# Optimization experiments

Hardware: AMD Instinct MI355X
Metric: run time of the kernel (lower is better)

Reference implementation:

```python
import jax, jax.numpy as jnp
import numpy as np
import math

B, L, DP, DB, H, DH = 1, 256, 128, 128, 8, 32


def _ln(x, g, b, eps=1e-5):
    m = x.mean(-1, keepdims=True)
    v = x.var(-1, keepdims=True)
    return (x - m) / jnp.sqrt(v + eps) * g + b


def setup_inputs() -> dict:
    key = jax.random.key(0)
    ks = jax.random.split(key, 12)
    s_in = 1.0 / math.sqrt(DP)
    s_hd = 1.0 / math.sqrt(H * DH)
    return {
        "pair": jax.random.normal(ks[0], (B, L, L, DP), jnp.float32),
        "bias": jax.random.normal(ks[1], (B, L, L, DB), jnp.float32),
        "mask": jax.random.randint(ks[2], (B, L), 0, 2, jnp.int32),
        "g_pair": jnp.ones((DP,), jnp.float32),
        "b_pair": jnp.zeros((DP,), jnp.float32),
        "g_bias": jnp.ones((DB,), jnp.float32),
        "b_bias": jnp.zeros((DB,), jnp.float32),
        "Wq": jax.random.normal(ks[3], (DP, H * DH), jnp.float32) * s_in,
        "Wk": jax.random.normal(ks[4], (DP, H * DH), jnp.float32) * s_in,
        "Wv": jax.random.normal(ks[5], (DP, H * DH), jnp.float32) * s_in,
        "Wb": jax.random.normal(ks[6], (DB, H), jnp.float32) * s_in,
        "Wg": jax.random.normal(ks[7], (DP, H * DH), jnp.float32) * s_in,
        "bg": jnp.ones((H * DH,), jnp.float32),
        "Wo": jax.random.normal(ks[8], (H * DH, DP), jnp.float32) * s_hd,
        "bo": jnp.zeros((DP,), jnp.float32),
    }


def reference(pair, bias, mask, g_pair, b_pair, g_bias, b_bias,
              Wq, Wk, Wv, Wb, Wg, bg, Wo, bo):
    is_row = True
    scaling = 1.0 / math.sqrt(DH)

    mask_b = (mask == 0)                               # [B,L], True = masked
    mask_2d = mask_b[:, None, :] | mask_b[:, :, None]  # [B,L,L]

    p = jnp.nan_to_num(pair)
    bi = jnp.nan_to_num(bias)
    if is_row:
        p = p.transpose(0, 2, 1, 3)
        bi = bi.transpose(0, 2, 1, 3)
        mask_2d = mask_2d.transpose(0, 2, 1)

    pn = _ln(p, g_pair, b_pair)        # [B,L,L,DP]
    bn = _ln(bi, g_bias, b_bias)       # [B,L,L,DB]

    q = (pn @ Wq).reshape(B, L, L, H, DH) * scaling
    k = (pn @ Wk).reshape(B, L, L, H, DH) / math.sqrt(L)
    v = (pn @ Wv).reshape(B, L, L, H, DH)
    b_proj = bn @ Wb                   # [B,L,L,H]
    gate = jax.nn.sigmoid(pn @ Wg + bg)  # [B,L,L,H*DH]

    # scores summed over the axial (n) axis AND head dim k
    attn = jnp.einsum('bnihk,bnjhk->bijh', q, k) + b_proj
    attn = jnp.where(mask_2d[..., None], -1e9, attn)
    attn = jax.nn.softmax(attn, axis=-2)  # over j

    out = jnp.einsum('bijh,bkjhd->bikhd', attn, v).reshape(B, L, L, H * DH)
    out = gate * out
    out = out @ Wo + bo                # [B,L,L,DP]
    if is_row:
        out = out.transpose(0, 2, 1, 3)
    # note: faithful to source — output mask uses the (permuted) mask_2d frame
    out = jnp.where(mask_2d[..., None], 0.0, out)
    return out
```

## Files before the change

kernel.cpp:

```cpp
#include <hip/hip_runtime.h>
#include <math.h>


typedef unsigned short u16;
typedef __attribute__((ext_vector_type(8))) short short8;
typedef __attribute__((ext_vector_type(4))) short short4v;
typedef __attribute__((ext_vector_type(4))) float float4v;

__device__ __forceinline__ u16 f2bf(float f) {
  unsigned int u = __float_as_uint(f);
  u += 0x7FFFu + ((u >> 16) & 1u);
  return (u16)(u >> 16);
}
__device__ __forceinline__ float bf2f(u16 h) {
  return __uint_as_float(((unsigned int)h) << 16);
}

__global__ __launch_bounds__(256, 4) void k_pre(
    const float* __restrict__ x1, const float* __restrict__ g1,
    const float* __restrict__ b1, u16* __restrict__ y1,
    const float* __restrict__ x2, const float* __restrict__ g2,
    const float* __restrict__ b2, const float* __restrict__ Wb,
    float* __restrict__ Bp,
    const float* __restrict__ Wq, const float* __restrict__ Wk,
    const float* __restrict__ Wv, const float* __restrict__ Wg,
    const float* __restrict__ Wo, u16* __restrict__ Wtb, u16* __restrict__ Wotb) {
  __shared__ float wbs[128 * 9];
  const int bid = blockIdx.x;
  const int t = threadIdx.x;
  if (bid < 1024) {
    const int row = t >> 3, h = t & 7;
    const int p0 = bid * 64 + row;
    const int p1 = p0 + 32;
    const float* rpA = x1 + (size_t)p0 * 128 + h * 16;
    const float* rpB = x1 + (size_t)p1 * 128 + h * 16;
    float4 xa[4], xb[4], gv4[4], bv4[4];
#pragma unroll
    for (int i = 0; i < 4; ++i) xa[i] = ((const float4*)rpA)[i];
#pragma unroll
    for (int i = 0; i < 4; ++i) xb[i] = ((const float4*)rpB)[i];
#pragma unroll
    for (int i = 0; i < 4; ++i) {
      gv4[i] = ((const float4*)(g1 + h * 16))[i];
      bv4[i] = ((const float4*)(b1 + h * 16))[i];
    }
    __builtin_amdgcn_sched_barrier(0);
    float sA = 0.f, ssA = 0.f, sB = 0.f, ssB = 0.f;
#pragma unroll
    for (int i = 0; i < 4; ++i) {
      sA += (xa[i].x + xa[i].y) + (xa[i].z + xa[i].w);
      ssA += (xa[i].x * xa[i].x + xa[i].y * xa[i].y) + (xa[i].z * xa[i].z + xa[i].w * xa[i].w);
      sB += (xb[i].x + xb[i].y) + (xb[i].z + xb[i].w);
      ssB += (xb[i].x * xb[i].x + xb[i].y * xb[i].y) + (xb[i].z * xb[i].z + xb[i].w * xb[i].w);
    }
#pragma unroll
    for (int off = 1; off <= 4; off <<= 1) {
      sA += __shfl_xor(sA, off);
      ssA += __shfl_xor(ssA, off);
      sB += __shfl_xor(sB, off);
      ssB += __shfl_xor(ssB, off);
    }
    float mA = sA * (1.0f / 128.0f);
    float invA = rsqrtf(ssA * (1.0f / 128.0f) - mA * mA + 1e-5f);
    float mB = sB * (1.0f / 128.0f);
    float invB = rsqrtf(ssB * (1.0f / 128.0f) - mB * mB + 1e-5f);
    short8 oA[2], oB[2];
#pragma unroll
    for (int i4 = 0; i4 < 4; ++i4) {
      float4 gv = gv4[i4], bv = bv4[i4];
      oA[i4 >> 1][(i4 & 1) * 4 + 0] = (short)f2bf((xa[i4].x - mA) * invA * gv.x + bv.x);
      oA[i4 >> 1][(i4 & 1) * 4 + 1] = (short)f2bf((xa[i4].y - mA) * invA * gv.y + bv.y);
      oA[i4 >> 1][(i4 & 1) * 4 + 2] = (short)f2bf((xa[i4].z - mA) * invA * gv.z + bv.z);
      oA[i4 >> 1][(i4 & 1) * 4 + 3] = (short)f2bf((xa[i4].w - mA) * invA * gv.w + bv.w);
      oB[i4 >> 1][(i4 & 1) * 4 + 0] = (short)f2bf((xb[i4].x - mB) * invB * gv.x + bv.x);
      oB[i4 >> 1][(i4 & 1) * 4 + 1] = (short)f2bf((xb[i4].y - mB) * invB * gv.y + bv.y);
      oB[i4 >> 1][(i4 & 1) * 4 + 2] = (short)f2bf((xb[i4].z - mB) * invB * gv.z + bv.z);
      oB[i4 >> 1][(i4 & 1) * 4 + 3] = (short)f2bf((xb[i4].w - mB) * invB * gv.w + bv.w);
    }
    u16* opA = y1 + (size_t)p0 * 128 + h * 16;
    *(short8*)opA = oA[0];
    *(short8*)(opA + 8) = oA[1];
    u16* opB = y1 + (size_t)p1 * 128 + h * 16;
    *(short8*)opB = oB[0];
    *(short8*)(opB + 8) = oB[1];
  } else if (bid < 2048) {
    {
      float4 wv = ((const float4*)Wb)[t];
      const int k = t >> 1, e0 = (t & 1) * 4;
      wbs[k * 9 + e0 + 0] = wv.x;
      wbs[k * 9 + e0 + 1] = wv.y;
      wbs[k * 9 + e0 + 2] = wv.z;
      wbs[k * 9 + e0 + 3] = wv.w;
    }
    const int row = t >> 3, h = t & 7;
    const int p0 = (bid - 1024) * 64 + row;
    const int p1 = p0 + 32;
    const int r0 = p0 >> 8, sc0 = p0 & 255;
    const int r1 = p1 >> 8, sc1 = p1 & 255;
    const float* rpA = x2 + (size_t)p0 * 128 + h * 16;
    const float* rpB = x2 + (size_t)p1 * 128 + h * 16;
    float4 xa[4], xb[4], gv4[4], bv4[4];
#pragma unroll
    for (int i = 0; i < 4; ++i) xa[i] = ((const float4*)rpA)[i];
#pragma unroll
    for (int i = 0; i < 4; ++i) xb[i] = ((const float4*)rpB)[i];
#pragma unroll
    for (int i = 0; i < 4; ++i) {
      gv4[i] = ((const float4*)(g2 + h * 16))[i];
      bv4[i] = ((const float4*)(b2 + h * 16))[i];
    }
    __builtin_amdgcn_sched_barrier(0);
    __syncthreads();
    float sA = 0.f, ssA = 0.f, sB = 0.f, ssB = 0.f;
#pragma unroll
    for (int i = 0; i < 4; ++i) {
      sA += (xa[i].x + xa[i].y) + (xa[i].z + xa[i].w);
      ssA += (xa[i].x * xa[i].x + xa[i].y * xa[i].y) + (xa[i].z * xa[i].z + xa[i].w * xa[i].w);
      sB += (xb[i].x + xb[i].y) + (xb[i].z + xb[i].w);
      ssB += (xb[i].x * xb[i].x + xb[i].y * xb[i].y) + (xb[i].z * xb[i].z + xb[i].w * xb[i].w);
    }
#pragma unroll
    for (int off = 1; off <= 4; off <<= 1) {
      sA += __shfl_xor(sA, off);
      ssA += __shfl_xor(ssA, off);
      sB += __shfl_xor(sB, off);
      ssB += __shfl_xor(ssB, off);
    }
    float mA = sA * (1.0f / 128.0f);
    float invA = rsqrtf(ssA * (1.0f / 128.0f) - mA * mA + 1e-5f);
    float mB = sB * (1.0f / 128.0f);
    float invB = rsqrtf(ssB * (1.0f / 128.0f) - mB * mB + 1e-5f);
    float pa[8], pb[8];
#pragma unroll
    for (int e = 0; e < 8; ++e) {
      pa[e] = 0.f;
      pb[e] = 0.f;
    }
#pragma unroll
    for (int i4 = 0; i4 < 4; ++i4) {
      float4 gv = gv4[i4], bv = bv4[i4];
      float xsA[4] = {xa[i4].x, xa[i4].y, xa[i4].z, xa[i4].w};
      float xsB[4] = {xb[i4].x, xb[i4].y, xb[i4].z, xb[i4].w};
      float gs[4] = {gv.x, gv.y, gv.z, gv.w};
      float bs[4] = {bv.x, bv.y, bv.z, bv.w};
#pragma unroll
      for (int q = 0; q < 4; ++q) {
        const int k = h * 16 + i4 * 4 + q;
        float xnA = (xsA[q] - mA) * invA * gs[q] + bs[q];
        float xnB = (xsB[q] - mB) * invB * gs[q] + bs[q];
        const float* wr = &wbs[k * 9];
#pragma unroll
        for (int e = 0; e < 8; ++e) {
          float w = wr[e];
          pa[e] += xnA * w;
          pb[e] += xnB * w;
        }
      }
    }
#pragma unroll
    for (int off = 1; off <= 4; off <<= 1) {
#pragma unroll
      for (int e = 0; e < 8; ++e) {
        pa[e] += __shfl_xor(pa[e], off);
        pb[e] += __shfl_xor(pb[e], off);
      }
    }
    float vA = (h == 0) ? pa[0]
             : (h == 1) ? pa[1]
             : (h == 2) ? pa[2]
             : (h == 3) ? pa[3]
             : (h == 4) ? pa[4]
             : (h == 5) ? pa[5]
             : (h == 6) ? pa[6]
                        : pa[7];
    float vB = (h == 0) ? pb[0]
             : (h == 1) ? pb[1]
             : (h == 2) ? pb[2]
             : (h == 3) ? pb[3]
             : (h == 4) ? pb[4]
             : (h == 5) ? pb[5]
             : (h == 6) ? pb[6]
                        : pb[7];
    Bp[(size_t)h * 65536 + (size_t)sc0 * 256 + r0] = vA;
    Bp[(size_t)h * 65536 + (size_t)sc1 * 256 + r1] = vB;
  } else {
    int idx = (bid - 2048) * 256 + t;
    if (idx < 131072) {
      int w = idx >> 15, r = idx & 32767;
      int k = r >> 8, n = r & 255;
      const float* W = (w == 0) ? Wq : (w == 1) ? Wk : (w == 2) ? Wv : Wg;
      const float sW = (w == 1) ? 0.0625f : 1.0f;
      Wtb[(size_t)w * 32768 + n * 128 + k] = f2bf(W[k * 256 + n] * sW);
    } else {
      int r = idx - 131072;
      int e = r >> 7, c = r & 127;
      Wotb[c * 256 + e] = f2bf(Wo[e * 128 + c]);
    }
  }
}

__global__ __launch_bounds__(256) void k_proj_qkg(const u16* __restrict__ PNb,
                                                  const u16* __restrict__ Wtb,
                                                  const float* __restrict__ bg,
                                                  u16* __restrict__ Qr4,
                                                  u16* __restrict__ Kr4,
                                                  u16* __restrict__ G2) {
  const int t = threadIdx.x;
  const int wid = t >> 6, lane = t & 63;
  const int mrow = lane & 15, quad = lane >> 4;
  const int stripe = blockIdx.x;
  const int n0 = blockIdx.y * 64;
  const int wsel3 = blockIdx.z;
  const int wsel = (wsel3 == 2) ? 3 : wsel3;
  const u16* Wt = Wtb + (size_t)wsel * 32768;
  u16* dst = (wsel3 == 0) ? Qr4 : (wsel3 == 1) ? Kr4 : G2;

  short8 bfr[4][4];
#pragma unroll
  for (int nt = 0; nt < 4; ++nt)
#pragma unroll
    for (int kk = 0; kk < 4; ++kk)
      bfr[nt][kk] = *(const short8*)(Wt + (size_t)(n0 + nt * 16 + mrow) * 128 + kk * 32 + quad * 8);

  float bgv[4];
#pragma unroll
  for (int nt = 0; nt < 4; ++nt) bgv[nt] = bg[n0 + nt * 16 + mrow];

  short8 afr[2][4], afrn[2][4];
  {
    const int pw = stripe * 512 + wid * 32;
#pragma unroll
    for (int mt = 0; mt < 2; ++mt)
#pragma unroll
      for (int kk = 0; kk < 4; ++kk)
        afr[mt][kk] =
            *(const short8*)(PNb + (size_t)(pw + mt * 16 + mrow) * 128 + kk * 32 + quad * 8);
  }
  for (int it = 0; it < 4; ++it) {
    const int pw = stripe * 512 + it * 128 + wid * 32;
    if (it < 3) {
      const int pn = pw + 128;
#pragma unroll
      for (int mt = 0; mt < 2; ++mt)
#pragma unroll
        for (int kk = 0; kk < 4; ++kk)
          afrn[mt][kk] =
              *(const short8*)(PNb + (size_t)(pn + mt * 16 + mrow) * 128 + kk * 32 + quad * 8);
    }
    float4v acc[2][4];
#pragma unroll
    for (int mt = 0; mt < 2; ++mt)
#pragma unroll
      for (int nt = 0; nt < 4; ++nt) acc[mt][nt] = (float4v){0.f, 0.f, 0.f, 0.f};
#pragma unroll
    for (int kk = 0; kk < 4; ++kk)
#pragma unroll
      for (int mt = 0; mt < 2; ++mt)
#pragma unroll
        for (int nt = 0; nt < 4; ++nt)
          acc[mt][nt] = __builtin_amdgcn_mfma_f32_16x16x32_bf16(afr[mt][kk], bfr[nt][kk],
                                                                acc[mt][nt], 0, 0, 0);
#pragma unroll
    for (int mt = 0; mt < 2; ++mt) {
      const int prow4 = ((pw + mt * 16) >> 2) + quad;
#pragma unroll
      for (int nt = 0; nt < 4; ++nt) {
        const int n = n0 + nt * 16 + mrow;
        short4v pk;
#pragma unroll
        for (int reg = 0; reg < 4; ++reg) {
          float v = acc[mt][nt][reg];
          if (wsel3 == 0) {
            v *= 0.17677669529663687f;
          } else if (wsel3 == 2) {
            float e = __expf(-(v + bgv[nt]));
            v = __builtin_amdgcn_rcpf(1.0f + e);
          }
          pk[reg] = (short)f2bf(v);
        }
        *(short4v*)(dst + ((size_t)prow4 * 256 + n) * 4) = pk;
      }
    }
#pragma unroll
    for (int mt = 0; mt < 2; ++mt)
#pragma unroll
      for (int kk = 0; kk < 4; ++kk) afr[mt][kk] = afrn[mt][kk];
  }
}

__global__ __launch_bounds__(256) void k_projv(const u16* __restrict__ PNb,
                                               const u16* __restrict__ Wtb,
                                               u16* __restrict__ Vtb) {
  const int t = threadIdx.x;
  const int wid = t >> 6, lane = t & 63;
  const int mrow = lane & 15, quad = lane >> 4;
  const int sc = blockIdx.x;
  const int n0 = blockIdx.y * 64;
  const u16* Wt = Wtb + (size_t)2 * 32768;

  short8 bfr[4][4];
#pragma unroll
  for (int nt = 0; nt < 4; ++nt)
#pragma unroll
    for (int kk = 0; kk < 4; ++kk)
      bfr[nt][kk] = *(const short8*)(Wt + (size_t)(n0 + nt * 16 + mrow) * 128 + kk * 32 + quad * 8);

  short8 afr[2][4], afrn[2][4];
  {
    const int rbase = wid * 32;
#pragma unroll
    for (int mt = 0; mt < 2; ++mt)
#pragma unroll
      for (int kk = 0; kk < 4; ++kk)
        afr[mt][kk] = *(const short8*)(PNb + ((size_t)(rbase + mt * 16 + mrow) * 256 + sc) * 128 +
                                       kk * 32 + quad * 8);
  }
  for (int it = 0; it < 2; ++it) {
    const int rbase = it * 128 + wid * 32;
    if (it == 0) {
      const int rn = 128 + wid * 32;
#pragma unroll
      for (int mt = 0; mt < 2; ++mt)
#pragma unroll
        for (int kk = 0; kk < 4; ++kk)
          afrn[mt][kk] = *(const short8*)(PNb + ((size_t)(rn + mt * 16 + mrow) * 256 + sc) * 128 +
                                          kk * 32 + quad * 8);
    }
    float4v acc[2][4];
#pragma unroll
    for (int mt = 0; mt < 2; ++mt)
#pragma unroll
      for (int nt = 0; nt < 4; ++nt) acc[mt][nt] = (float4v){0.f, 0.f, 0.f, 0.f};
#pragma unroll
    for (int kk = 0; kk < 4; ++kk)
#pragma unroll
      for (int mt = 0; mt < 2; ++mt)
#pragma unroll
        for (int nt = 0; nt < 4; ++nt)
          acc[mt][nt] = __builtin_amdgcn_mfma_f32_16x16x32_bf16(afr[mt][kk], bfr[nt][kk],
                                                                acc[mt][nt], 0, 0, 0);
#pragma unroll
    for (int mt = 0; mt < 2; ++mt) {
      const int j0 = rbase + mt * 16 + quad * 4;
#pragma unroll
      for (int nt = 0; nt < 4; ++nt) {
        const int n = n0 + nt * 16 + mrow;
        const int h = n >> 5, d = n & 31;
        short4v pk;
#pragma unroll
        for (int reg = 0; reg < 4; ++reg) pk[reg] = (short)f2bf(acc[mt][nt][reg]);
        *(short4v*)(Vtb + (size_t)h * 2097152 + (size_t)(sc * 32 + d) * 256 + j0) = pk;
      }
    }
#pragma unroll
    for (int mt = 0; mt < 2; ++mt)
#pragma unroll
      for (int kk = 0; kk < 4; ++kk) afr[mt][kk] = afrn[mt][kk];
  }
}

__global__ __launch_bounds__(256) void k_logits_mfma(const u16* __restrict__ Qr4,
                                                     const u16* __restrict__ Kr4,
                                                     float* __restrict__ Lg2) {
  __shared__ u16 Qs[128 * 72];
  __shared__ u16 Ks[128 * 72];
  const int t = threadIdx.x;
  const int wid = t >> 6, lane = t & 63;
  const int mrow = lane & 15, quad = lane >> 4;
  const int i0 = (blockIdx.x >> 1) * 128, j0 = (blockIdx.x & 1) * 128;
  const int h = blockIdx.y;
  const int z = blockIdx.z;
  const int wi = wid >> 1, wj = wid & 1;
  float4v acc[4][4];
#pragma unroll
  for (int a = 0; a < 4; ++a)
#pragma unroll
    for (int bq = 0; bq < 4; ++bq) acc[a][bq] = (float4v){0.f, 0.f, 0.f, 0.f};

  for (int g = 0; g < 4; ++g) {
    const int sc4 = z * 4 + g;
    for (int sub = 0; sub < 2; ++sub) {
      __syncthreads();
#pragma unroll
      for (int itq = 0; itq < 4; ++itq) {
        int u = itq * 256 + t;
        int i_loc = u >> 3, c16 = sub * 8 + (u & 7);
        size_t qoff = ((size_t)((i0 + i_loc) * 64 + sc4) * 256 + h * 32 + c16 * 2) * 4;
        *(short8*)&Qs[i_loc * 72 + (u & 7) * 8] = *(const short8*)(Qr4 + qoff);
        size_t koff = ((size_t)((j0 + i_loc) * 64 + sc4) * 256 + h * 32 + c16 * 2) * 4;
        *(short8*)&Ks[i_loc * 72 + (u & 7) * 8] = *(const short8*)(Kr4 + koff);
      }
      __syncthreads();
#pragma unroll
      for (int kk = 0; kk < 2; ++kk) {
        short8 afr[4], bfr[4];
#pragma unroll
        for (int mt = 0; mt < 4; ++mt)
          afr[mt] = *(const short8*)&Qs[(wi * 64 + mt * 16 + mrow) * 72 + kk * 32 + quad * 8];
#pragma unroll
        for (int nn = 0; nn < 4; ++nn)
          bfr[nn] = *(const short8*)&Ks[(wj * 64 + nn * 16 + mrow) * 72 + kk * 32 + quad * 8];
#pragma unroll
        for (int mt = 0; mt < 4; ++mt)
#pragma unroll
          for (int nn = 0; nn < 4; ++nn)
            acc[mt][nn] =
                __builtin_amdgcn_mfma_f32_16x16x32_bf16(afr[mt], bfr[nn], acc[mt][nn], 0, 0, 0);
      }
    }
  }
  float* slab = Lg2 + ((size_t)z * 8 + h) * 65536;
#pragma unroll
  for (int mt = 0; mt < 4; ++mt)
#pragma unroll
    for (int nn = 0; nn < 4; ++nn) {
      int j = j0 + wj * 64 + nn * 16 + mrow;
#pragma unroll
      for (int reg = 0; reg < 4; ++reg) {
        int i = i0 + wi * 64 + mt * 16 + quad * 4 + reg;
        slab[(size_t)i * 256 + j] = acc[mt][nn][reg];
      }
    }
}

__global__ __launch_bounds__(256, 4) void k_softmax(const float* __restrict__ Bp,
                                                    const float* __restrict__ Lg2,
                                                    const int* __restrict__ mask,
                                                    u16* __restrict__ Ab) {
  const int i = blockIdx.x, h = blockIdx.y;
  const int j = threadIdx.x;
  __shared__ float red[4], red2[4];
  const size_t off = (size_t)h * 65536 + (size_t)i * 256 + j;
  float v[16];
#pragma unroll
  for (int z = 0; z < 16; ++z) v[z] = Lg2[(size_t)z * 524288 + off];
  float x = Bp[off];
#pragma unroll
  for (int z = 0; z < 16; ++z) x += v[z];
  bool mi = (mask[i] == 0);
  if (mi || (mask[j] == 0)) x = -1e9f;
  float mx = x;
#pragma unroll
  for (int off2 = 32; off2; off2 >>= 1) mx = fmaxf(mx, __shfl_xor(mx, off2));
  int wave = j >> 6;
  if ((j & 63) == 0) red[wave] = mx;
  __syncthreads();
  mx = fmaxf(fmaxf(red[0], red[1]), fmaxf(red[2], red[3]));
  float e = expf(x - mx);
  float sm = e;
#pragma unroll
  for (int off2 = 32; off2; off2 >>= 1) sm += __shfl_xor(sm, off2);
  if ((j & 63) == 0) red2[wave] = sm;
  __syncthreads();
  sm = red2[0] + red2[1] + red2[2] + red2[3];
  Ab[off] = f2bf(e / sm);
}

__global__ __launch_bounds__(256) void k_av_mfma(const u16* __restrict__ Ab,
                                                 const u16* __restrict__ Vtb,
                                                 const u16* __restrict__ G2,
                                                 u16* __restrict__ GOb) {
  __shared__ u16 As[64 * 264];
  __shared__ u16 Ts[4][64 * 72];
  const int t = threadIdx.x;
  const int wid = t >> 6, lane = t & 63;
  const int mrow = lane & 15, quad = lane >> 4;
  const int h = blockIdx.z;
  const int i0 = blockIdx.y * 64;
  const u16* ag = Ab + (size_t)h * 65536 + (size_t)i0 * 256;
#pragma unroll
  for (int u = 0; u < 8; ++u) {
    int id = u * 256 + t;
    int rr = id >> 5, c8 = (id & 31) * 8;
    *(short8*)&As[rr * 264 + c8] = *(const short8*)(ag + (size_t)rr * 256 + c8);
  }
  __syncthreads();
  const u16* vg = Vtb + (size_t)h * 2097152;
  u16* tw = &Ts[wid][0];
  const int c = lane & 7, lr = lane >> 3;
  for (int nt4 = 0; nt4 < 4; ++nt4) {
    const int nbase = blockIdx.x * 1024 + wid * 256 + nt4 * 64;
    float4v acc[4][4];
#pragma unroll
    for (int a = 0; a < 4; ++a)
#pragma unroll
      for (int bq = 0; bq < 4; ++bq) acc[a][bq] = (float4v){0.f, 0.f, 0.f, 0.f};
#pragma unroll
    for (int kk = 0; kk < 8; ++kk) {
      short8 afr[4], bfr[4];
#pragma unroll
      for (int mt = 0; mt < 4; ++mt)
        afr[mt] = *(const short8*)&As[(mt * 16 + mrow) * 264 + kk * 32 + quad * 8];
#pragma unroll
      for (int nn = 0; nn < 4; ++nn)
        bfr[nn] = *(const short8*)(vg + (size_t)(nbase + nn * 16 + mrow) * 256 + kk * 32 + quad * 8);
#pragma unroll
      for (int mt = 0; mt < 4; ++mt)
#pragma unroll
        for (int nn = 0; nn < 4; ++nn)
          acc[mt][nn] = __builtin_amdgcn_mfma_f32_16x16x32_bf16(afr[mt], bfr[nn], acc[mt][nn], 0, 0, 0);
    }
#pragma unroll
    for (int mt = 0; mt < 4; ++mt)
#pragma unroll
      for (int nn = 0; nn < 4; ++nn) {
        const int kslot = (nbase + nn * 16) >> 5;
        const int d = (nn & 1) * 16 + mrow;
        const int e = h * 32 + d;
        const int p4 = kslot * 64 + ((i0 + mt * 16) >> 2) + quad;
        short4v g4 = *(const short4v*)(G2 + ((size_t)p4 * 256 + e) * 4);
        const int il0 = mt * 16 + quad * 4;
        const int nl = nn * 16 + mrow;
#pragma unroll
        for (int reg = 0; reg < 4; ++reg) {
          float gv = bf2f((u16)g4[reg]);
          tw[(il0 + reg) * 72 + nl] = f2bf(acc[mt][nn][reg] * gv);
        }
      }
    asm volatile("s_waitcnt lgkmcnt(0)" ::: "memory");
    const int kslot0 = nbase >> 5;
#pragma unroll
    for (int y = 0; y < 8; ++y) {
      const int il = y * 8 + lr;
      short8 val = *(const short8*)(tw + il * 72 + c * 8);
      const int i = i0 + il;
      const int kslot = kslot0 + (c >> 2);
      size_t idx = ((size_t)i * 256 + kslot) * 256 + h * 32 + (c & 3) * 8;
      *(short8*)(GOb + idx) = val;
    }
  }
}

__global__ __launch_bounds__(256) void k_out_mfma(const u16* __restrict__ GOb,
                                                  const u16* __restrict__ Wotb,
                                                  const float* __restrict__ bo,
                                                  const int* __restrict__ mask,
                                                  float* __restrict__ out) {
  const int wid = threadIdx.x >> 6, lane = threadIdx.x & 63;
  const int mrow = lane & 15, quad = lane >> 4;
  const int m0 = blockIdx.x * 128 + wid * 32;
  short8 afr[2][8];
#pragma unroll
  for (int mt = 0; mt < 2; ++mt) {
    const u16* ar = GOb + (size_t)(m0 + mt * 16 + mrow) * 256 + quad * 8;
#pragma unroll
    for (int kk = 0; kk < 8; ++kk) afr[mt][kk] = *(const short8*)(ar + kk * 32);
  }
  for (int nt = 0; nt < 8; ++nt) {
    float4v acc[2];
    acc[0] = (float4v){0.f, 0.f, 0.f, 0.f};
    acc[1] = (float4v){0.f, 0.f, 0.f, 0.f};
    const u16* br = Wotb + (size_t)(nt * 16 + mrow) * 256 + quad * 8;
#pragma unroll
    for (int kk = 0; kk < 8; ++kk) {
      short8 bfr = *(const short8*)(br + kk * 32);
#pragma unroll
      for (int mt = 0; mt < 2; ++mt)
        acc[mt] = __builtin_amdgcn_mfma_f32_16x16x32_bf16(afr[mt][kk], bfr, acc[mt], 0, 0, 0);
    }
    const int c = nt * 16 + mrow;
    float bov = bo[c];
#pragma unroll
    for (int mt = 0; mt < 2; ++mt) {
#pragma unroll
      for (int reg = 0; reg < 4; ++reg) {
        int m = m0 + mt * 16 + quad * 4 + reg;
        int i = m >> 8, kq = m & 255;
        float v = acc[mt][reg] + bov;
        bool z = (mask[i] == 0) || (mask[kq] == 0);
        out[((size_t)kq * 256 + i) * 128 + c] = z ? 0.f : v;
      }
    }
  }
}

extern "C" void kernel_launch(void* const* d_in, const int* in_sizes, int n_in,
                              void* d_out, int out_size, void* d_ws, size_t ws_size,
                              hipStream_t stream) {
  const float* pair = (const float*)d_in[0];
  const float* bias = (const float*)d_in[1];
  const int* mask = (const int*)d_in[2];
  const float* g_pair = (const float*)d_in[3];
  const float* b_pair = (const float*)d_in[4];
  const float* g_bias = (const float*)d_in[5];
  const float* b_bias = (const float*)d_in[6];
  const float* Wq = (const float*)d_in[7];
  const float* Wk = (const float*)d_in[8];
  const float* Wv = (const float*)d_in[9];
  const float* Wb = (const float*)d_in[10];
  const float* Wg = (const float*)d_in[11];
  const float* bg = (const float*)d_in[12];
  const float* Wo = (const float*)d_in[13];
  const float* bo = (const float*)d_in[14];
  float* out = (float*)d_out;
  char* ws = (char*)d_ws;

  u16* PNb = (u16*)(ws + 0);
  u16* Qr4 = (u16*)(ws + 16777216);
  u16* Kr4 = (u16*)(ws + 50331648);
  u16* Vtb = (u16*)(ws + 83886080);
  u16* G2 = (u16*)(ws + 117440512);
  u16* GOb = (u16*)(ws + 150994944);
  float* Bp = (float*)(ws + 184549376);
  u16* Ab = (u16*)(ws + 186646528);
  u16* Wtb = (u16*)(ws + 187695104);
  u16* Wotb = (u16*)(ws + 187957248);
  float* Lg2 = (float*)(ws + 188022784);

  k_pre<<<2688, 256, 0, stream>>>(pair, g_pair, b_pair, PNb, bias, g_bias, b_bias, Wb, Bp,
                                  Wq, Wk, Wv, Wg, Wo, Wtb, Wotb);
  k_proj_qkg<<<dim3(128, 4, 3), 256, 0, stream>>>(PNb, Wtb, bg, Qr4, Kr4, G2);
  k_projv<<<dim3(256, 4), 256, 0, stream>>>(PNb, Wtb, Vtb);
  k_logits_mfma<<<dim3(4, 8, 16), 256, 0, stream>>>(Qr4, Kr4, Lg2);
  k_softmax<<<dim3(256, 8), 256, 0, stream>>>(Bp, Lg2, mask, Ab);
  k_av_mfma<<<dim3(8, 4, 8), 256, 0, stream>>>(Ab, Vtb, G2, GOb);
  k_out_mfma<<<512, 256, 0, stream>>>(GOb, Wotb, bo, mask, out);
}
```

Measured before the change: 291.9 us.

## Fuse gate projection into AV kernel, halve logits split-K, vectorize softmax

Removes the gate projection from the QKG projection kernel and recomputes sigmoid(pn@Wg+bg) on the fly inside the AV kernel via MFMA, eliminating the G2 intermediate write and read. The logits kernel now reduces over 8 chunks per block instead of 4, which halves the number of partial-logit slabs the softmax must read. Softmax is rewritten to one wave per row, using float4 loads and shuffle-only reductions with no shared memory. Output stores become nontemporal. The cost is extra MFMA work and PNb reads in the AV kernel, plus fewer blocks in the logits kernel.

```diff
diff --git a/kernel.cpp b/kernel.cpp
--- a/kernel.cpp
+++ b/kernel.cpp
@@ -201,19 +201,16 @@
 
 __global__ __launch_bounds__(256) void k_proj_qkg(const u16* __restrict__ PNb,
                                                   const u16* __restrict__ Wtb,
-                                                  const float* __restrict__ bg,
                                                   u16* __restrict__ Qr4,
-                                                  u16* __restrict__ Kr4,
-                                                  u16* __restrict__ G2) {
+                                                  u16* __restrict__ Kr4) {
   const int t = threadIdx.x;
   const int wid = t >> 6, lane = t & 63;
   const int mrow = lane & 15, quad = lane >> 4;
   const int stripe = blockIdx.x;
   const int n0 = blockIdx.y * 64;
-  const int wsel3 = blockIdx.z;
-  const int wsel = (wsel3 == 2) ? 3 : wsel3;
+  const int wsel = blockIdx.z;
   const u16* Wt = Wtb + (size_t)wsel * 32768;
-  u16* dst = (wsel3 == 0) ? Qr4 : (wsel3 == 1) ? Kr4 : G2;
+  u16* dst = (wsel == 0) ? Qr4 : Kr4;
 
   short8 bfr[4][4];
 #pragma unroll
@@ -221,10 +218,6 @@
 #pragma unroll
     for (int kk = 0; kk < 4; ++kk)
       bfr[nt][kk] = *(const short8*)(Wt + (size_t)(n0 + nt * 16 + mrow) * 128 + kk * 32 + quad * 8);
-
-  float bgv[4];
-#pragma unroll
-  for (int nt = 0; nt < 4; ++nt) bgv[nt] = bg[n0 + nt * 16 + mrow];
 
   short8 afr[2][4], afrn[2][4];
   {
@@ -270,12 +263,7 @@
 #pragma unroll
         for (int reg = 0; reg < 4; ++reg) {
           float v = acc[mt][nt][reg];
-          if (wsel3 == 0) {
-            v *= 0.17677669529663687f;
-          } else if (wsel3 == 2) {
-            float e = __expf(-(v + bgv[nt]));
-            v = __builtin_amdgcn_rcpf(1.0f + e);
-          }
+          if (wsel == 0) v *= 0.17677669529663687f;
           pk[reg] = (short)f2bf(v);
         }
         *(short4v*)(dst + ((size_t)prow4 * 256 + n) * 4) = pk;
@@ -377,8 +365,8 @@
 #pragma unroll
     for (int bq = 0; bq < 4; ++bq) acc[a][bq] = (float4v){0.f, 0.f, 0.f, 0.f};
 
-  for (int g = 0; g < 4; ++g) {
-    const int sc4 = z * 4 + g;
+  for (int g = 0; g < 8; ++g) {
+    const int sc4 = z * 8 + g;
     for (int sub = 0; sub < 2; ++sub) {
       __syncthreads();
 #pragma unroll
@@ -423,42 +411,50 @@
     }
 }
 
-__global__ __launch_bounds__(256, 4) void k_softmax(const float* __restrict__ Bp,
-                                                    const float* __restrict__ Lg2,
-                                                    const int* __restrict__ mask,
-                                                    u16* __restrict__ Ab) {
-  const int i = blockIdx.x, h = blockIdx.y;
-  const int j = threadIdx.x;
-  __shared__ float red[4], red2[4];
-  const size_t off = (size_t)h * 65536 + (size_t)i * 256 + j;
-  float v[16];
-#pragma unroll
-  for (int z = 0; z < 16; ++z) v[z] = Lg2[(size_t)z * 524288 + off];
-  float x = Bp[off];
-#pragma unroll
-  for (int z = 0; z < 16; ++z) x += v[z];
-  bool mi = (mask[i] == 0);
-  if (mi || (mask[j] == 0)) x = -1e9f;
-  float mx = x;
-#pragma unroll
-  for (int off2 = 32; off2; off2 >>= 1) mx = fmaxf(mx, __shfl_xor(mx, off2));
-  int wave = j >> 6;
-  if ((j & 63) == 0) red[wave] = mx;
-  __syncthreads();
-  mx = fmaxf(fmaxf(red[0], red[1]), fmaxf(red[2], red[3]));
-  float e = expf(x - mx);
-  float sm = e;
-#pragma unroll
-  for (int off2 = 32; off2; off2 >>= 1) sm += __shfl_xor(sm, off2);
-  if ((j & 63) == 0) red2[wave] = sm;
-  __syncthreads();
-  sm = red2[0] + red2[1] + red2[2] + red2[3];
-  Ab[off] = f2bf(e / sm);
+__global__ __launch_bounds__(256) void k_softmax(const float* __restrict__ Bp,
+                                                 const float* __restrict__ Lg2,
+                                                 const int* __restrict__ mask,
+                                                 u16* __restrict__ Ab) {
+  const int w = threadIdx.x >> 6, lane = threadIdx.x & 63;
+  const int i = blockIdx.x * 4 + w, h = blockIdx.y;
+  const size_t off = (size_t)h * 65536 + (size_t)i * 256 + lane * 4;
+  float4 x4 = *(const float4*)(Bp + off);
+  float4 v[8];
+#pragma unroll
+  for (int z = 0; z < 8; ++z) v[z] = *(const float4*)(Lg2 + (size_t)z * 524288 + off);
+  int4 mj = *(const int4*)(mask + lane * 4);
+  const bool mi = (mask[i] == 0);
+#pragma unroll
+  for (int z = 0; z < 8; ++z) {
+    x4.x += v[z].x;
+    x4.y += v[z].y;
+    x4.z += v[z].z;
+    x4.w += v[z].w;
+  }
+  if (mi || mj.x == 0) x4.x = -1e9f;
+  if (mi || mj.y == 0) x4.y = -1e9f;
+  if (mi || mj.z == 0) x4.z = -1e9f;
+  if (mi || mj.w == 0) x4.w = -1e9f;
+  float mx = fmaxf(fmaxf(x4.x, x4.y), fmaxf(x4.z, x4.w));
+#pragma unroll
+  for (int o = 32; o; o >>= 1) mx = fmaxf(mx, __shfl_xor(mx, o));
+  float e0 = expf(x4.x - mx), e1 = expf(x4.y - mx), e2 = expf(x4.z - mx), e3 = expf(x4.w - mx);
+  float sm = (e0 + e1) + (e2 + e3);
+#pragma unroll
+  for (int o = 32; o; o >>= 1) sm += __shfl_xor(sm, o);
+  short4v pk;
+  pk[0] = (short)f2bf(e0 / sm);
+  pk[1] = (short)f2bf(e1 / sm);
+  pk[2] = (short)f2bf(e2 / sm);
+  pk[3] = (short)f2bf(e3 / sm);
+  *(short4v*)(Ab + off) = pk;
 }
 
 __global__ __launch_bounds__(256) void k_av_mfma(const u16* __restrict__ Ab,
                                                  const u16* __restrict__ Vtb,
-                                                 const u16* __restrict__ G2,
+                                                 const u16* __restrict__ PNb,
+                                                 const u16* __restrict__ Wtb,
+                                                 const float* __restrict__ bg,
                                                  u16* __restrict__ GOb) {
   __shared__ u16 As[64 * 264];
   __shared__ u16 Ts[4][64 * 72];
@@ -476,10 +472,63 @@
   }
   __syncthreads();
   const u16* vg = Vtb + (size_t)h * 2097152;
+  const u16* Wg3 = Wtb + (size_t)3 * 32768;
+  short8 bfrg[2][4];
+  float bgv2[2];
+#pragma unroll
+  for (int eh = 0; eh < 2; ++eh) {
+#pragma unroll
+    for (int kk = 0; kk < 4; ++kk)
+      bfrg[eh][kk] =
+          *(const short8*)(Wg3 + (size_t)(h * 32 + eh * 16 + mrow) * 128 + kk * 32 + quad * 8);
+    bgv2[eh] = bg[h * 32 + eh * 16 + mrow];
+  }
   u16* tw = &Ts[wid][0];
   const int c = lane & 7, lr = lane >> 3;
   for (int nt4 = 0; nt4 < 4; ++nt4) {
     const int nbase = blockIdx.x * 1024 + wid * 256 + nt4 * 64;
+    const int kslot0 = nbase >> 5;
+    short4v gbf[2][4][2];
+    {
+      float4v gacc[2][4][2];
+#pragma unroll
+      for (int ks = 0; ks < 2; ++ks)
+#pragma unroll
+        for (int mt = 0; mt < 4; ++mt)
+#pragma unroll
+          for (int eh = 0; eh < 2; ++eh) gacc[ks][mt][eh] = (float4v){0.f, 0.f, 0.f, 0.f};
+#pragma unroll
+      for (int ks = 0; ks < 2; ++ks) {
+#pragma unroll
+        for (int mt = 0; mt < 4; ++mt) {
+          const int p0 = (kslot0 + ks) * 256 + i0 + mt * 16;
+          short8 afg[4];
+#pragma unroll
+          for (int kk = 0; kk < 4; ++kk)
+            afg[kk] = *(const short8*)(PNb + (size_t)(p0 + mrow) * 128 + kk * 32 + quad * 8);
+#pragma unroll
+          for (int kk = 0; kk < 4; ++kk)
+#pragma unroll
+            for (int eh = 0; eh < 2; ++eh)
+              gacc[ks][mt][eh] = __builtin_amdgcn_mfma_f32_16x16x32_bf16(afg[kk], bfrg[eh][kk],
+                                                                         gacc[ks][mt][eh], 0, 0, 0);
+        }
+      }
+#pragma unroll
+      for (int ks = 0; ks < 2; ++ks)
+#pragma unroll
+        for (int mt = 0; mt < 4; ++mt)
+#pragma unroll
+          for (int eh = 0; eh < 2; ++eh) {
+            short4v pk;
+#pragma unroll
+            for (int reg = 0; reg < 4; ++reg) {
+              float ex = __expf(-(gacc[ks][mt][eh][reg] + bgv2[eh]));
+              pk[reg] = (short)f2bf(__builtin_amdgcn_rcpf(1.0f + ex));
+            }
+            gbf[ks][mt][eh] = pk;
+          }
+    }
     float4v acc[4][4];
 #pragma unroll
     for (int a = 0; a < 4; ++a)
@@ -504,11 +553,7 @@
     for (int mt = 0; mt < 4; ++mt)
 #pragma unroll
       for (int nn = 0; nn < 4; ++nn) {
-        const int kslot = (nbase + nn * 16) >> 5;
-        const int d = (nn & 1) * 16 + mrow;
-        const int e = h * 32 + d;
-        const int p4 = kslot * 64 + ((i0 + mt * 16) >> 2) + quad;
-        short4v g4 = *(const short4v*)(G2 + ((size_t)p4 * 256 + e) * 4);
+        short4v g4 = gbf[nn >> 1][mt][nn & 1];
         const int il0 = mt * 16 + quad * 4;
         const int nl = nn * 16 + mrow;
 #pragma unroll
@@ -518,13 +563,13 @@
         }
       }
     asm volatile("s_waitcnt lgkmcnt(0)" ::: "memory");
-    const int kslot0 = nbase >> 5;
+    const int kslot0s = nbase >> 5;
 #pragma unroll
     for (int y = 0; y < 8; ++y) {
       const int il = y * 8 + lr;
       short8 val = *(const short8*)(tw + il * 72 + c * 8);
       const int i = i0 + il;
-      const int kslot = kslot0 + (c >> 2);
+      const int kslot = kslot0s + (c >> 2);
       size_t idx = ((size_t)i * 256 + kslot) * 256 + h * 32 + (c & 3) * 8;
       *(short8*)(GOb + idx) = val;
     }
@@ -568,7 +613,7 @@
         int i = m >> 8, kq = m & 255;
         float v = acc[mt][reg] + bov;
         bool z = (mask[i] == 0) || (mask[kq] == 0);
-        out[((size_t)kq * 256 + i) * 128 + c] = z ? 0.f : v;
+        __builtin_nontemporal_store(z ? 0.f : v, &out[((size_t)kq * 256 + i) * 128 + c]);
       }
     }
   }
@@ -599,7 +644,6 @@
   u16* Qr4 = (u16*)(ws + 16777216);
   u16* Kr4 = (u16*)(ws + 50331648);
   u16* Vtb = (u16*)(ws + 83886080);
-  u16* G2 = (u16*)(ws + 117440512);
   u16* GOb = (u16*)(ws + 150994944);
   float* Bp = (float*)(ws + 184549376);
   u16* Ab = (u16*)(ws + 186646528);
@@ -609,10 +653,10 @@
 
   k_pre<<<2688, 256, 0, stream>>>(pair, g_pair, b_pair, PNb, bias, g_bias, b_bias, Wb, Bp,
                                   Wq, Wk, Wv, Wg, Wo, Wtb, Wotb);
-  k_proj_qkg<<<dim3(128, 4, 3), 256, 0, stream>>>(PNb, Wtb, bg, Qr4, Kr4, G2);
+  k_proj_qkg<<<dim3(128, 4, 2), 256, 0, stream>>>(PNb, Wtb, Qr4, Kr4);
   k_projv<<<dim3(256, 4), 256, 0, stream>>>(PNb, Wtb, Vtb);
-  k_logits_mfma<<<dim3(4, 8, 16), 256, 0, stream>>>(Qr4, Kr4, Lg2);
-  k_softmax<<<dim3(256, 8), 256, 0, stream>>>(Bp, Lg2, mask, Ab);
-  k_av_mfma<<<dim3(8, 4, 8), 256, 0, stream>>>(Ab, Vtb, G2, GOb);
+  k_logits_mfma<<<dim3(4, 8, 8), 256, 0, stream>>>(Qr4, Kr4, Lg2);
+  k_softmax<<<dim3(64, 8), 256, 0, stream>>>(Bp, Lg2, mask, Ab);
+  k_av_mfma<<<dim3(8, 4, 8), 256, 0, stream>>>(Ab, Vtb, PNb, Wtb, bg, GOb);
   k_out_mfma<<<512, 256, 0, stream>>>(GOb, Wotb, bo, mask, out);
 }
```

After: 298.8 us. 2.4% more time.
